# Kernel optimization log

Measured on AMD Instinct MI355X. Metric: run time of the kernel, lower is better.

## Reference

```python
import jax, jax.numpy as jnp
import numpy as np

N, M, B, L, C, H = 4096, 16384, 8, 96, 512, 8
Dh = C // H


def setup_inputs() -> dict:
    key0 = jax.random.key(0)
    ks = jax.random.split(key0, 8)
    query = jax.random.normal(ks[0], (N, C), dtype=jnp.float32)
    key_t = jax.random.normal(ks[1], (M, C), dtype=jnp.float32)
    value = jax.random.normal(ks[2], (M, C), dtype=jnp.float32)
    keys_per_batch = M // B  # 2048 local key indices per scene
    idx = jax.random.randint(ks[3], (N, L), 0, keys_per_batch)
    pad = jax.random.uniform(ks[4], (N, L)) < 0.1
    pad = pad.at[:, 0].set(False)
    index_pair = jnp.where(pad, -1, idx).astype(jnp.int64)
    query_batch_cnt = jnp.full((B,), N // B, dtype=jnp.int32)
    key_batch_cnt = jnp.full((B,), M // B, dtype=jnp.int32)
    index_pair_batch = jnp.repeat(jnp.arange(B, dtype=jnp.int64), N // B)
    in_proj_weight = jax.random.normal(ks[5], (3 * C, C), dtype=jnp.float32) * (1.0 / np.sqrt(C))
    in_proj_bias = jnp.zeros((3 * C,), dtype=jnp.float32)
    out_proj_weight = jax.random.normal(ks[6], (C, C), dtype=jnp.float32) * (1.0 / np.sqrt(C))
    out_proj_bias = jnp.zeros((C,), dtype=jnp.float32)
    return {
        "query": query, "key": key_t, "value": value,
        "index_pair": index_pair, "query_batch_cnt": query_batch_cnt,
        "key_batch_cnt": key_batch_cnt, "index_pair_batch": index_pair_batch,
        "in_proj_weight": in_proj_weight, "in_proj_bias": in_proj_bias,
        "out_proj_weight": out_proj_weight, "out_proj_bias": out_proj_bias,
    }


def reference(query, key, value, index_pair, query_batch_cnt, key_batch_cnt,
              index_pair_batch, in_proj_weight, in_proj_bias,
              out_proj_weight, out_proj_bias):
    n, c = query.shape
    l = index_pair.shape[1]
    scaling = float(Dh) ** -0.5
    # QKV projections (F.linear: x @ W.T + b)
    q = query @ in_proj_weight[:c].T + in_proj_bias[:c]
    k = key @ in_proj_weight[c:2 * c].T + in_proj_bias[c:2 * c]
    v = value @ in_proj_weight[2 * c:].T + in_proj_bias[2 * c:]
    q = (q * scaling).reshape(n, H, Dh)
    k = k.reshape(-1, H, Dh)
    v = v.reshape(-1, H, Dh)
    mask = index_pair < 0  # (N, L)
    # convert local per-batch key index to global index via exclusive cumsum of key counts
    offs = jnp.concatenate([jnp.zeros((1,), key_batch_cnt.dtype), jnp.cumsum(key_batch_cnt)[:-1]])
    gidx = jnp.where(mask, 0, index_pair + offs[index_pair_batch][:, None])  # (N, L)
    k_g = k[gidx]  # (N, L, H, Dh)
    attn = jnp.einsum('nhd,nlhd->nlh', q, k_g)
    attn = jnp.where(mask[:, :, None], -jnp.inf, attn)
    attn = jax.nn.softmax(attn, axis=1)  # softmax over neighbor dim L
    v_g = v[gidx]  # (N, L, H, Dh)
    out = jnp.einsum('nlh,nlhd->nhd', attn, v_g).reshape(n, c)
    out = out @ out_proj_weight.T + out_proj_bias
    return out, attn.sum(axis=-1) / H
```

## Files before the change

### kernel.cpp

```cpp
#include <hip/hip_runtime.h>
#include <hip/hip_fp16.h>
#include <cstdint>
#include <cstddef>

#define N_Q 4096
#define M_K 16384
#define LNB 96
#define CH  512
#define NH  8

typedef _Float16 half8  __attribute__((ext_vector_type(8)));
typedef _Float16 h2     __attribute__((ext_vector_type(2)));
typedef float    floatx4 __attribute__((ext_vector_type(4)));
typedef float    floatx2 __attribute__((ext_vector_type(2)));

union H8 { half8 v; h2 p[4]; };

__device__ __forceinline__ h2 cvt2(float a, float b) {
    return __builtin_bit_cast(h2, __builtin_amdgcn_cvt_pkrtz(a, b));
}

__device__ __forceinline__ void async16(const void* g, void* l) {
    __builtin_amdgcn_global_load_lds(
        (const __attribute__((address_space(1))) void*)g,
        (__attribute__((address_space(3))) void*)l, 16, 0, 0);
}

template<int CTRL>
__device__ __forceinline__ float dpp_addf(float x) {
    int xi = __builtin_bit_cast(int, x);
    int yi = __builtin_amdgcn_update_dpp(xi, xi, CTRL, 0xF, 0xF, false);
    return x + __builtin_bit_cast(float, yi);
}
__device__ __forceinline__ float octet_sum(float x) {
    x = dpp_addf<0x141>(x);
    x = dpp_addf<0x4E>(x);
    x = dpp_addf<0xB1>(x);
    return x;
}

__global__ void cvt_weights(const float* __restrict__ wIn, const float* __restrict__ wOut,
                            _Float16* __restrict__ dst) {
    const size_t i = (size_t)blockIdx.x * blockDim.x + threadIdx.x;
    const float4 v = (i < 196608) ? ((const float4*)wIn)[i]
                                  : ((const float4*)wOut)[i - 196608];
    h2 a = cvt2(v.x, v.y);
    h2 b = cvt2(v.z, v.w);
    *(h2*)&dst[i * 4]     = a;
    *(h2*)&dst[i * 4 + 2] = b;
}

template<int OUTF16, int TM, int AFP32>
__device__ __forceinline__ void gemm_body(
    const void* __restrict__ Ap, const _Float16* __restrict__ Bw,
    const float* __restrict__ bias, void* __restrict__ outp, float oscale,
    int bm, int bn)
{
    constexpr int MI = TM / 32;
    __shared__ alignas(16) _Float16 As[TM * 32];
    __shared__ alignas(16) _Float16 Bs[128 * 32];

    const int t    = threadIdx.x;
    const int lane = t & 63;
    const int wave = t >> 6;
    const int wm   = wave >> 1, wn = wave & 1;

    floatx4 acc[MI][4] = {};

    const int rowL = t >> 2;
    const int kcol = (t & 3) * 8;
    const _Float16* gB = Bw + (size_t)(bn * 128 + rowL) * CH + kcol;
    _Float16* lB = &Bs[rowL * 32 + kcol];

    const _Float16* gA16 = nullptr; _Float16* lA16 = nullptr;
    const float* gA32 = nullptr; _Float16* lA32 = nullptr;
    if constexpr (AFP32) {
        gA32 = (const float*)Ap + (size_t)(bm * TM + rowL) * CH + kcol;
        lA32 = &As[rowL * 32 + kcol];
    } else {
        gA16 = (const _Float16*)Ap + (size_t)(bm * TM + rowL) * CH + kcol;
        lA16 = &As[rowL * 32 + kcol];
    }

    const int r0 = lane & 15;
    const int ko = (lane >> 4) * 8;

    for (int kt = 0; kt < CH / 32; ++kt) {
        if constexpr (AFP32) {
            const float* ga = gA32 + kt * 32;
            float4 x0 = ((const float4*)ga)[0], x1 = ((const float4*)ga)[1];
            H8 o0;
            o0.p[0] = cvt2(x0.x, x0.y);
            o0.p[1] = cvt2(x0.z, x0.w);
            o0.p[2] = cvt2(x1.x, x1.y);
            o0.p[3] = cvt2(x1.z, x1.w);
            *(half8*)lA32 = o0.v;
        } else {
            const _Float16* a0 = gA16 + kt * 32;
            async16(a0, lA16);
        }
        const _Float16* b0 = gB + kt * 32;
        async16(b0,           lB);
        async16(b0 + 64 * CH, lB + 64 * 32);
        __syncthreads();

        half8 af[MI], bf[4];
        #pragma unroll
        for (int mi = 0; mi < MI; ++mi)
            af[mi] = *(const half8*)&As[(wm * (TM / 2) + mi * 16 + r0) * 32 + ko];
        #pragma unroll
        for (int ni = 0; ni < 4; ++ni)
            bf[ni] = *(const half8*)&Bs[(wn * 64 + ni * 16 + r0) * 32 + ko];
        #pragma unroll
        for (int mi = 0; mi < MI; ++mi)
            #pragma unroll
            for (int ni = 0; ni < 4; ++ni)
                acc[mi][ni] = __builtin_amdgcn_mfma_f32_16x16x32_f16(
                    af[mi], bf[ni], acc[mi][ni], 0, 0, 0);
        __syncthreads();
    }

    #pragma unroll
    for (int mi = 0; mi < MI; ++mi) {
        #pragma unroll
        for (int ni = 0; ni < 4; ++ni) {
            const int col = bn * 128 + wn * 64 + ni * 16 + (lane & 15);
            const float bv = bias[col];
            #pragma unroll
            for (int r = 0; r < 4; ++r) {
                const int row = bm * TM + wm * (TM / 2) + mi * 16 + (lane >> 4) * 4 + r;
                const float v = (acc[mi][ni][r] + bv) * oscale;
                if (OUTF16) ((_Float16*)outp)[(size_t)row * CH + col] = (_Float16)v;
                else        ((float*)outp)[(size_t)row * CH + col]    = v;
            }
        }
    }
}

template<int OUTF16, int TM, int AFP32>
__global__ __launch_bounds__(256) void gemm_k(
    const void* __restrict__ A, const _Float16* __restrict__ Bw,
    const float* __restrict__ bias, void* __restrict__ outp, float oscale)
{
    const int bid = blockIdx.x;
    const int x   = bid & 7;
    const int i   = bid >> 3;
    const int bn  = i & 3;
    const int bm  = x + 8 * (i >> 2);
    gemm_body<OUTF16, TM, AFP32>(A, Bw, bias, outp, oscale, bm, bn);
}

__global__ __launch_bounds__(256) void gemm_kv(
    const float* __restrict__ keyp, const float* __restrict__ valp,
    const _Float16* __restrict__ w16, const float* __restrict__ bIn,
    _Float16* __restrict__ k16, _Float16* __restrict__ v16)
{
    const int bid = blockIdx.x;
    const int x   = bid & 7;
    const int i   = bid >> 3;
    const int bn  = i & 3;
    const int z   = (i >> 2) & 1;
    const int bm  = x + 8 * (i >> 3);

    const char*     Ab   = (const char*)(z ? valp : keyp);
    const char*     Bb   = (const char*)(w16 + (size_t)(z ? 1024 : 512) * 512);
    const float*    bias = bIn + (z ? 1024 : 512);
    _Float16*       outp = z ? v16 : k16;

    __shared__ alignas(16) float    As[128 * 32];
    __shared__ alignas(16) _Float16 Bs[128 * 32];

    const int t    = threadIdx.x;
    const int lane = t & 63;
    const int wave = t >> 6;
    const int wm   = wave >> 1, wn = wave & 1;

    floatx4 acc[4][4] = {};

    uint32_t aoff[4]; char* alds[4];
    #pragma unroll
    for (int q = 0; q < 4; ++q) {
        const int G   = q * 256 + t;
        const int row = G >> 3;
        const int g   = (G & 7) ^ (row & 7);
        aoff[q] = (uint32_t)((bm * 128 + row) * 2048 + g * 16);
        alds[q] = (char*)As + (size_t)G * 16;
    }
    uint32_t boff[2]; char* blds[2];
    #pragma unroll
    for (int q = 0; q < 2; ++q) {
        const int G     = q * 256 + t;
        const int super = G >> 3;
        const int sgg   = (G & 7) ^ (super & 7);
        const int row   = super * 2 + (sgg >> 2);
        const int g     = sgg & 3;
        boff[q] = (uint32_t)((bn * 128 + row) * 1024 + g * 16);
        blds[q] = (char*)Bs + (size_t)G * 16;
    }

    const int r0  = lane & 15;
    const int hi  = lane >> 4;
    const int swz = r0 & 7;

    for (int kt = 0; kt < 16; ++kt) {
        #pragma unroll
        for (int q = 0; q < 4; ++q) async16(Ab + aoff[q] + kt * 128, alds[q]);
        #pragma unroll
        for (int q = 0; q < 2; ++q) async16(Bb + boff[q] + kt * 64, blds[q]);
        __syncthreads();

        half8 af[4], bf[4];
        #pragma unroll
        for (int mi = 0; mi < 4; ++mi) {
            const int row = wm * 64 + mi * 16 + r0;
            const float4 x0 = *(const float4*)((const char*)As + row * 128 + (((hi * 2)     ^ swz) * 16));
            const float4 x1 = *(const float4*)((const char*)As + row * 128 + (((hi * 2 + 1) ^ swz) * 16));
            H8 o;
            o.p[0] = cvt2(x0.x, x0.y);
            o.p[1] = cvt2(x0.z, x0.w);
            o.p[2] = cvt2(x1.x, x1.y);
            o.p[3] = cvt2(x1.z, x1.w);
            af[mi] = o.v;
        }
        #pragma unroll
        for (int ni = 0; ni < 4; ++ni) {
            const int row   = wn * 64 + ni * 16 + r0;
            const int super = row >> 1;
            const int vv    = ((row & 1) * 4 + hi) ^ (super & 7);
            bf[ni] = *(const half8*)((const char*)Bs + super * 128 + vv * 16);
        }
        #pragma unroll
        for (int mi = 0; mi < 4; ++mi)
            #pragma unroll
            for (int ni = 0; ni < 4; ++ni)
                acc[mi][ni] = __builtin_amdgcn_mfma_f32_16x16x32_f16(
                    af[mi], bf[ni], acc[mi][ni], 0, 0, 0);
        __syncthreads();
    }

    #pragma unroll
    for (int mi = 0; mi < 4; ++mi) {
        #pragma unroll
        for (int ni = 0; ni < 4; ++ni) {
            const int col = bn * 128 + wn * 64 + ni * 16 + (lane & 15);
            const float bv = bias[col];
            #pragma unroll
            for (int r = 0; r < 4; ++r) {
                const int row = bm * 128 + wm * 64 + mi * 16 + (lane >> 4) * 4 + r;
                outp[(size_t)row * CH + col] = (_Float16)(acc[mi][ni][r] + bv);
            }
        }
    }
}

__global__ __launch_bounds__(256) void attn_kernel(
    const _Float16* __restrict__ q16, const _Float16* __restrict__ k16,
    const _Float16* __restrict__ v16, const int* __restrict__ ipair,
    const int* __restrict__ ibatch, const int* __restrict__ kcnt,
    _Float16* __restrict__ op16, float* __restrict__ aout)
{
    __shared__ uint32_t vmask[LNB];
    __shared__ float    pls[LNB * 9];
    __shared__ __half2  pph[LNB * 9];
    __shared__ float    part[4][CH];

    const int t = threadIdx.x;
    const int n = ((blockIdx.x & 7) << 9) | (blockIdx.x >> 3);

    if (t < LNB) {
        const int idx = ipair[(size_t)n * LNB + t];
        const int b   = ibatch[n];
        int off = 0;
        for (int i = 0; i < b; ++i) off += kcnt[i];
        const uint32_t vo = (uint32_t)((idx < 0 ? 0 : (idx + off)) * (CH * 2));
        vmask[t] = vo | (idx < 0 ? 0x80000000u : 0u);
    }
    __syncthreads();

    const int lane = t & 63, wv = t >> 6;
    const int h    = lane >> 3;
    const int l0   = wv * 24;

    {
        const half8 qv = *(const half8*)(q16 + (size_t)n * CH + lane * 8);
        H8 qu; qu.v = qv;
        const char* kbase = (const char*)k16 + lane * 16;
        const int4* vb = (const int4*)&vmask[l0];
        for (int g = 0; g < 3; ++g) {
            const int4 w0 = vb[2 * g], w1 = vb[2 * g + 1];
            uint32_t vm8[8] = {(uint32_t)w0.x, (uint32_t)w0.y, (uint32_t)w0.z, (uint32_t)w0.w,
                               (uint32_t)w1.x, (uint32_t)w1.y, (uint32_t)w1.z, (uint32_t)w1.w};
            #pragma unroll
            for (int j = 0; j < 8; ++j) {
                const uint32_t vms = __builtin_amdgcn_readfirstlane(vm8[j]);
                H8 ku; ku.v = *(const half8*)(kbase + (vms & 0x7fffffffu));
                float acc = 0.f;
                #pragma unroll
                for (int u = 0; u < 4; ++u)
                    acc = __builtin_amdgcn_fdot2(qu.p[u], ku.p[u], acc, false);
                acc = octet_sum(acc);
                if ((lane & 7) == 0)
                    pls[(l0 + g * 8 + j) * 9 + h] = (vms & 0x80000000u) ? -1e30f : acc;
            }
        }
    }
    __syncthreads();

    {
        const int hh = t >> 5, j = t & 31;
        const float v0 = pls[j * 9 + hh];
        const float v1 = pls[(j + 32) * 9 + hh];
        const float v2 = pls[(j + 64) * 9 + hh];
        float m = fmaxf(v0, fmaxf(v1, v2));
        #pragma unroll
        for (int s = 16; s >= 1; s >>= 1) m = fmaxf(m, __shfl_xor(m, s, 32));
        const float e0 = __expf(v0 - m), e1 = __expf(v1 - m), e2 = __expf(v2 - m);
        float ssum = e0 + e1 + e2;
        #pragma unroll
        for (int s = 16; s >= 1; s >>= 1) ssum += __shfl_xor(ssum, s, 32);
        const float rinv = 1.0f / ssum;
        const float p0 = e0 * rinv, p1 = e1 * rinv, p2 = e2 * rinv;
        pls[j * 9 + hh]        = p0;
        pls[(j + 32) * 9 + hh] = p1;
        pls[(j + 64) * 9 + hh] = p2;
        pph[j * 9 + hh]        = __half2half2(__float2half_rn(p0));
        pph[(j + 32) * 9 + hh] = __half2half2(__float2half_rn(p1));
        pph[(j + 64) * 9 + hh] = __half2half2(__float2half_rn(p2));
    }
    __syncthreads();

    if (t < LNB) {
        float s = 0.f;
        #pragma unroll
        for (int u = 0; u < NH; ++u) s += pls[t * 9 + u];
        aout[(size_t)n * LNB + t] = s * (1.0f / NH);
    }

    {
        float accf[8] = {};
        const char* vbase = (const char*)v16 + lane * 16;
        const int4* vb = (const int4*)&vmask[l0];
        const __half2 hz = __half2half2(__float2half_rn(0.f));
        for (int g = 0; g < 3; ++g) {
            const int4 w0 = vb[2 * g], w1 = vb[2 * g + 1];
            uint32_t vm8[8] = {(uint32_t)w0.x, (uint32_t)w0.y, (uint32_t)w0.z, (uint32_t)w0.w,
                               (uint32_t)w1.x, (uint32_t)w1.y, (uint32_t)w1.z, (uint32_t)w1.w};
            __half2 a0 = hz, a1 = hz, a2 = hz, a3 = hz;
            #pragma unroll
            for (int j = 0; j < 8; ++j) {
                const uint32_t vms = __builtin_amdgcn_readfirstlane(vm8[j]);
                const half8 vv = *(const half8*)(vbase + (vms & 0x7fffffffu));
                union { half8 v; __half2 q[4]; } vu; vu.v = vv;
                const __half2 pp = pph[(l0 + g * 8 + j) * 9 + h];
                a0 = __hfma2(pp, vu.q[0], a0);
                a1 = __hfma2(pp, vu.q[1], a1);
                a2 = __hfma2(pp, vu.q[2], a2);
                a3 = __hfma2(pp, vu.q[3], a3);
            }
            float2 f;
            f = __half22float2(a0); accf[0] += f.x; accf[1] += f.y;
            f = __half22float2(a1); accf[2] += f.x; accf[3] += f.y;
            f = __half22float2(a2); accf[4] += f.x; accf[5] += f.y;
            f = __half22float2(a3); accf[6] += f.x; accf[7] += f.y;
        }
        floatx4 lo, hi;
        #pragma unroll
        for (int u = 0; u < 4; ++u) { lo[u] = accf[u]; hi[u] = accf[u + 4]; }
        *(floatx4*)&part[wv][lane * 8]     = lo;
        *(floatx4*)&part[wv][lane * 8 + 4] = hi;
    }
    __syncthreads();

    {
        const int c = t * 2;
        floatx2 s = *(const floatx2*)&part[0][c];
        #pragma unroll
        for (int w = 1; w < 4; ++w) {
            floatx2 pw = *(const floatx2*)&part[w][c];
            s[0] += pw[0]; s[1] += pw[1];
        }
        h2 o; o[0] = (_Float16)s[0]; o[1] = (_Float16)s[1];
        *(h2*)&op16[(size_t)n * CH + c] = o;
    }
}

extern "C" void kernel_launch(void* const* d_in, const int* in_sizes, int n_in,
                              void* d_out, int out_size, void* d_ws, size_t ws_size,
                              hipStream_t stream)
{
    const float* query = (const float*)d_in[0];
    const float* key   = (const float*)d_in[1];
    const float* value = (const float*)d_in[2];
    const int*   ipair = (const int*)d_in[3];
    const int*   kcnt  = (const int*)d_in[5];
    const int*   ibat  = (const int*)d_in[6];
    const float* wIn   = (const float*)d_in[7];
    const float* bIn   = (const float*)d_in[8];
    const float* wOut  = (const float*)d_in[9];
    const float* bOut  = (const float*)d_in[10];

    float* out  = (float*)d_out;
    float* aout = out + (size_t)N_Q * CH;

    char* ws = (char*)d_ws;
    _Float16* w16  = (_Float16*)(ws);
    _Float16* wo16 = (_Float16*)(ws + 1572864);
    _Float16* q16  = (_Float16*)(ws + 2097152);
    _Float16* k16  = (_Float16*)(ws + 6291456);
    _Float16* v16  = (_Float16*)(ws + 23068672);
    _Float16* op16 = (_Float16*)(ws + 39845888);

    cvt_weights<<<1024, 256, 0, stream>>>(wIn, wOut, w16);

    gemm_k<1, 64, 1><<<256, 256, 0, stream>>>(query, w16, bIn, q16, 0.125f);

    gemm_kv<<<1024, 256, 0, stream>>>(key, value, w16, bIn, k16, v16);

    attn_kernel<<<4096, 256, 0, stream>>>(q16, k16, v16, ipair, ibat, kcnt, op16, aout);

    gemm_k<0, 64, 0><<<256, 256, 0, stream>>>(op16, wo16, bOut, d_out, 1.0f);
}
```

Baseline: 100.7 us.

## Load K/V GEMM operands directly from global into registers, drop LDS staging

The K/V projection GEMM no longer stages A and B tiles through shared memory with async global-to-LDS copies and barriers. Each lane now reads its MFMA fragments straight from global memory into registers, and the loop is unrolled by two so loads can overlap compute. This removes the LDS traffic and both __syncthreads per k-step. In exchange, each tile is read from global/L2 by both waves that share it instead of once, with 64-byte strided per-lane accesses that coalesce less well.

```diff
diff --git a/kernel.cpp b/kernel.cpp
--- a/kernel.cpp
+++ b/kernel.cpp
@@ -162,72 +162,46 @@
     const int z   = (i >> 2) & 1;
     const int bm  = x + 8 * (i >> 3);
 
-    const char*     Ab   = (const char*)(z ? valp : keyp);
-    const char*     Bb   = (const char*)(w16 + (size_t)(z ? 1024 : 512) * 512);
+    const float*    Af   = z ? valp : keyp;
+    const _Float16* Bw   = w16 + (size_t)(z ? 1024 : 512) * 512;
     const float*    bias = bIn + (z ? 1024 : 512);
     _Float16*       outp = z ? v16 : k16;
-
-    __shared__ alignas(16) float    As[128 * 32];
-    __shared__ alignas(16) _Float16 Bs[128 * 32];
 
     const int t    = threadIdx.x;
     const int lane = t & 63;
     const int wave = t >> 6;
     const int wm   = wave >> 1, wn = wave & 1;
+    const int r0   = lane & 15;
+    const int hi   = lane >> 4;
 
     floatx4 acc[4][4] = {};
 
-    uint32_t aoff[4]; char* alds[4];
-    #pragma unroll
-    for (int q = 0; q < 4; ++q) {
-        const int G   = q * 256 + t;
-        const int row = G >> 3;
-        const int g   = (G & 7) ^ (row & 7);
-        aoff[q] = (uint32_t)((bm * 128 + row) * 2048 + g * 16);
-        alds[q] = (char*)As + (size_t)G * 16;
-    }
-    uint32_t boff[2]; char* blds[2];
-    #pragma unroll
-    for (int q = 0; q < 2; ++q) {
-        const int G     = q * 256 + t;
-        const int super = G >> 3;
-        const int sgg   = (G & 7) ^ (super & 7);
-        const int row   = super * 2 + (sgg >> 2);
-        const int g     = sgg & 3;
-        boff[q] = (uint32_t)((bn * 128 + row) * 1024 + g * 16);
-        blds[q] = (char*)Bs + (size_t)G * 16;
-    }
-
-    const int r0  = lane & 15;
-    const int hi  = lane >> 4;
-    const int swz = r0 & 7;
-
+    const float4* gA = (const float4*)(Af + (size_t)(bm * 128 + wm * 64 + r0) * CH) + hi * 2;
+    const int4*   gB = (const int4*)(Bw + (size_t)(bn * 128 + wn * 64 + r0) * CH) + hi;
+
+    #pragma unroll 2
     for (int kt = 0; kt < 16; ++kt) {
-        #pragma unroll
-        for (int q = 0; q < 4; ++q) async16(Ab + aoff[q] + kt * 128, alds[q]);
-        #pragma unroll
-        for (int q = 0; q < 2; ++q) async16(Bb + boff[q] + kt * 64, blds[q]);
-        __syncthreads();
+        float4 a[4][2];
+        int4   b[4];
+        #pragma unroll
+        for (int mi = 0; mi < 4; ++mi) {
+            a[mi][0] = gA[mi * 2048 + kt * 8];
+            a[mi][1] = gA[mi * 2048 + kt * 8 + 1];
+        }
+        #pragma unroll
+        for (int ni = 0; ni < 4; ++ni)
+            b[ni] = gB[ni * 1024 + kt * 4];
 
         half8 af[4], bf[4];
         #pragma unroll
         for (int mi = 0; mi < 4; ++mi) {
-            const int row = wm * 64 + mi * 16 + r0;
-            const float4 x0 = *(const float4*)((const char*)As + row * 128 + (((hi * 2)     ^ swz) * 16));
-            const float4 x1 = *(const float4*)((const char*)As + row * 128 + (((hi * 2 + 1) ^ swz) * 16));
             H8 o;
-            o.p[0] = cvt2(x0.x, x0.y);
-            o.p[1] = cvt2(x0.z, x0.w);
-            o.p[2] = cvt2(x1.x, x1.y);
-            o.p[3] = cvt2(x1.z, x1.w);
+            o.p[0] = cvt2(a[mi][0].x, a[mi][0].y);
+            o.p[1] = cvt2(a[mi][0].z, a[mi][0].w);
+            o.p[2] = cvt2(a[mi][1].x, a[mi][1].y);
+            o.p[3] = cvt2(a[mi][1].z, a[mi][1].w);
             af[mi] = o.v;
-        }
-        #pragma unroll
-        for (int ni = 0; ni < 4; ++ni) {
-            const int row   = wn * 64 + ni * 16 + r0;
-            const int super = row >> 1;
-            const int vv    = ((row & 1) * 4 + hi) ^ (super & 7);
-            bf[ni] = *(const half8*)((const char*)Bs + super * 128 + vv * 16);
+            bf[mi] = __builtin_bit_cast(half8, b[mi]);
         }
         #pragma unroll
         for (int mi = 0; mi < 4; ++mi)
@@ -235,7 +209,6 @@
             for (int ni = 0; ni < 4; ++ni)
                 acc[mi][ni] = __builtin_amdgcn_mfma_f32_16x16x32_f16(
                     af[mi], bf[ni], acc[mi][ni], 0, 0, 0);
-        __syncthreads();
     }
 
     #pragma unroll
```

New measurement: 169.7 us. 68.4% more time.

## Fuse Q and KV projections into one kernel with 128x256 tiles

Applied to the files above, without the earlier changes.

Merges the separate Q projection GEMM and the K/V projection GEMM into a single launch of 576 blocks of 512 threads. Each block now computes a 128x256 output tile instead of 128x128, so every A tile is converted and reused across twice as many output columns, and one kernel launch and its tail are removed. The cost is twice the LDS for the B tile and larger blocks, which may reduce occupancy. The grid also gets a mixed workload, with Q blocks appended after the K/V blocks.

```diff
diff --git a/kernel.cpp b/kernel.cpp
--- a/kernel.cpp
+++ b/kernel.cpp
@@ -150,69 +150,90 @@
     gemm_body<OUTF16, TM, AFP32>(A, Bw, bias, outp, oscale, bm, bn);
 }
 
-__global__ __launch_bounds__(256) void gemm_kv(
-    const float* __restrict__ keyp, const float* __restrict__ valp,
-    const _Float16* __restrict__ w16, const float* __restrict__ bIn,
+__global__ __launch_bounds__(512, 4) void proj_qkv(
+    const float* __restrict__ query, const float* __restrict__ keyp,
+    const float* __restrict__ valp, const _Float16* __restrict__ w16,
+    const float* __restrict__ bIn, _Float16* __restrict__ q16,
     _Float16* __restrict__ k16, _Float16* __restrict__ v16)
 {
     const int bid = blockIdx.x;
-    const int x   = bid & 7;
-    const int i   = bid >> 3;
-    const int bn  = i & 3;
-    const int z   = (i >> 2) & 1;
-    const int bm  = x + 8 * (i >> 3);
-
-    const char*     Ab   = (const char*)(z ? valp : keyp);
-    const char*     Bb   = (const char*)(w16 + (size_t)(z ? 1024 : 512) * 512);
-    const float*    bias = bIn + (z ? 1024 : 512);
-    _Float16*       outp = z ? v16 : k16;
+    const float* Af; const _Float16* W; const float* bias; _Float16* dst;
+    float osc; int bm, cb;
+
+    if (bid < 512) {
+        const int x = bid & 7;
+        const int i = bid >> 3;
+        const int bn = i & 3;
+        bm = x + 8 * (i >> 2);
+        const int z = bn >> 1;
+        cb = (bn & 1) * 256;
+        Af   = z ? valp : keyp;
+        W    = w16 + (size_t)(512 + bn * 256) * 512;
+        bias = bIn + 512 + bn * 256;
+        dst  = z ? v16 : k16;
+        osc  = 1.0f;
+    } else {
+        const int x = bid & 7;
+        const int j = (bid - 512) >> 3;
+        const int bn = j & 1;
+        bm = x + 8 * (j >> 1);
+        cb = bn * 256;
+        Af   = query;
+        W    = w16 + (size_t)(bn * 256) * 512;
+        bias = bIn + bn * 256;
+        dst  = q16;
+        osc  = 0.125f;
+    }
 
     __shared__ alignas(16) float    As[128 * 32];
-    __shared__ alignas(16) _Float16 Bs[128 * 32];
+    __shared__ alignas(16) _Float16 Bs[256 * 32];
+
+    const char* Ab = (const char*)Af;
+    const char* Bb = (const char*)W;
 
     const int t    = threadIdx.x;
     const int lane = t & 63;
-    const int wave = t >> 6;
-    const int wm   = wave >> 1, wn = wave & 1;
+    const int wv   = t >> 6;
+    const int wm   = wv >> 2;
+    const int wn   = wv & 3;
+    const int r0   = lane & 15;
+    const int hi   = lane >> 4;
 
     floatx4 acc[4][4] = {};
 
-    uint32_t aoff[4]; char* alds[4];
+    uint32_t aoff[2];
     #pragma unroll
-    for (int q = 0; q < 4; ++q) {
-        const int G   = q * 256 + t;
+    for (int q = 0; q < 2; ++q) {
+        const int G   = q * 512 + t;
         const int row = G >> 3;
         const int g   = (G & 7) ^ (row & 7);
         aoff[q] = (uint32_t)((bm * 128 + row) * 2048 + g * 16);
-        alds[q] = (char*)As + (size_t)G * 16;
-    }
-    uint32_t boff[2]; char* blds[2];
+    }
+    uint32_t boff[2];
     #pragma unroll
     for (int q = 0; q < 2; ++q) {
-        const int G     = q * 256 + t;
+        const int G     = q * 512 + t;
         const int super = G >> 3;
         const int sgg   = (G & 7) ^ (super & 7);
         const int row   = super * 2 + (sgg >> 2);
         const int g     = sgg & 3;
-        boff[q] = (uint32_t)((bn * 128 + row) * 1024 + g * 16);
-        blds[q] = (char*)Bs + (size_t)G * 16;
-    }
-
-    const int r0  = lane & 15;
-    const int hi  = lane >> 4;
-    const int swz = r0 & 7;
+        boff[q] = (uint32_t)(row * 1024 + g * 16);
+    }
 
     for (int kt = 0; kt < 16; ++kt) {
         #pragma unroll
-        for (int q = 0; q < 4; ++q) async16(Ab + aoff[q] + kt * 128, alds[q]);
-        #pragma unroll
-        for (int q = 0; q < 2; ++q) async16(Bb + boff[q] + kt * 64, blds[q]);
+        for (int q = 0; q < 2; ++q)
+            async16(Ab + aoff[q] + kt * 128, (char*)As + (q * 512 + t) * 16);
+        #pragma unroll
+        for (int q = 0; q < 2; ++q)
+            async16(Bb + boff[q] + kt * 64,  (char*)Bs + (q * 512 + t) * 16);
         __syncthreads();
 
         half8 af[4], bf[4];
         #pragma unroll
         for (int mi = 0; mi < 4; ++mi) {
             const int row = wm * 64 + mi * 16 + r0;
+            const int swz = row & 7;
             const float4 x0 = *(const float4*)((const char*)As + row * 128 + (((hi * 2)     ^ swz) * 16));
             const float4 x1 = *(const float4*)((const char*)As + row * 128 + (((hi * 2 + 1) ^ swz) * 16));
             H8 o;
@@ -242,12 +263,13 @@
     for (int mi = 0; mi < 4; ++mi) {
         #pragma unroll
         for (int ni = 0; ni < 4; ++ni) {
-            const int col = bn * 128 + wn * 64 + ni * 16 + (lane & 15);
-            const float bv = bias[col];
+            const int lc  = wn * 64 + ni * 16 + r0;
+            const int col = cb + lc;
+            const float bv = bias[lc];
             #pragma unroll
             for (int r = 0; r < 4; ++r) {
-                const int row = bm * 128 + wm * 64 + mi * 16 + (lane >> 4) * 4 + r;
-                outp[(size_t)row * CH + col] = (_Float16)(acc[mi][ni][r] + bv);
+                const int row = bm * 128 + wm * 64 + mi * 16 + hi * 4 + r;
+                dst[(size_t)row * CH + col] = (_Float16)((acc[mi][ni][r] + bv) * osc);
             }
         }
     }
@@ -412,9 +434,7 @@
 
     cvt_weights<<<1024, 256, 0, stream>>>(wIn, wOut, w16);
 
-    gemm_k<1, 64, 1><<<256, 256, 0, stream>>>(query, w16, bIn, q16, 0.125f);
-
-    gemm_kv<<<1024, 256, 0, stream>>>(key, value, w16, bIn, k16, v16);
+    proj_qkv<<<576, 512, 0, stream>>>(query, key, value, w16, bIn, q16, k16, v16);
 
     attn_kernel<<<4096, 256, 0, stream>>>(q16, k16, v16, ipair, ibat, kcnt, op16, aout);
 
```

Result: faster. 97.33 us (-3.4%).
